# Optimization experiments

Hardware: AMD Instinct MI355X
Metric: run time of the kernel (lower is better)

## Reference

```python
import jax, jax.numpy as jnp
import numpy as np

EPS = 1e-8
MASK_FILL = 1000000000.0  # value used to disable dropped codes


def _normalize(x):
    return x / (jnp.linalg.norm(x, ord=2, axis=-1, keepdims=True) + EPS)


def setup_inputs() -> dict:
    key = jax.random.key(0)
    k_x, k_cb, k_mask = jax.random.split(key, 3)
    B, K, D = 16384, 16384, 64
    dropout = 0.1
    x = jax.random.normal(k_x, (B, D), dtype=jnp.float32)
    # lecun_uniform init for the codebook param: U(-l, l), l = sqrt(3 / fan_in)
    lim = np.sqrt(3.0 / D).astype(np.float32)
    codebook = jax.random.uniform(k_cb, (K, D), dtype=jnp.float32, minval=-lim, maxval=lim)
    mask = jax.random.bernoulli(k_mask, p=1.0 - dropout, shape=(B, K))
    return {"x": x, "codebook": codebook, "mask": mask, "training": 1}


def reference(x, codebook, mask, training):
    # setup(): codebook param is normalized once at construction
    cb = _normalize(codebook)                       # [K, d]
    # __call__():
    x_n = _normalize(x)                             # [b, d]
    cb_n = _normalize(cb)                           # normalized again in __call__
    distance = -jnp.matmul(x_n, cb_n.T)             # [b, K] negative cosine sim
    if training:
        distance = jnp.where(mask, distance, MASK_FILL)
    indices = jnp.argmin(distance, axis=-1)         # [b]
    z = cb[indices]                                 # gather from once-normalized codebook
    z_q = x_n + jax.lax.stop_gradient(z - x_n)      # straight-through estimator
    return (z_q, z, x_n, indices)
```

## Files before the change

### kernel.cpp

```cpp
#include <hip/hip_runtime.h>
#include <math.h>
#include <float.h>

#define EPSV 1e-8f
constexpr int D = 64;

typedef __attribute__((ext_vector_type(8)))  short short8;
typedef __attribute__((ext_vector_type(16))) float f32x16;

static __device__ __forceinline__ unsigned short f2bf(float f) {
    unsigned u = __float_as_uint(f);
    unsigned r = u + 0x7FFFu + ((u >> 16) & 1u);
    return (unsigned short)(r >> 16);
}
static __device__ __forceinline__ float bf2f(unsigned short b) {
    return __uint_as_float(((unsigned)b) << 16);
}
static __device__ __forceinline__ unsigned umin2(unsigned a, unsigned b) { return a < b ? a : b; }
static __device__ __forceinline__ unsigned umax2(unsigned a, unsigned b) { return a > b ? a : b; }

static __device__ __forceinline__ size_t fragidx(int e, int k) {
    return (size_t)(e >> 5) * 2048 + (size_t)(k >> 3) * 256 + (e & 31) * 8 + (k & 7);
}

__global__ __launch_bounds__(256) void k_prep(const float* __restrict__ cbin,
                                              float* __restrict__ cb,
                                              unsigned short* __restrict__ ch,
                                              unsigned short* __restrict__ cl,
                                              const float* __restrict__ xin,
                                              float* __restrict__ xn,
                                              unsigned short* __restrict__ xh,
                                              unsigned short* __restrict__ xl,
                                              int* __restrict__ fixcnt,
                                              int nbcb) {
    const int t = threadIdx.x;
    if (blockIdx.x == 0 && t == 0) *fixcnt = 0;
    const int wv = t >> 6, lane = t & 63;
    if ((int)blockIdx.x < nbcb) {
        const int code = blockIdx.x * 4 + wv;
        float v = cbin[(size_t)code * D + lane];
        float ss = v * v;
        #pragma unroll
        for (int off = 32; off; off >>= 1) ss += __shfl_xor(ss, off, 64);
        const float c1 = v / (sqrtf(ss) + EPSV);
        cb[(size_t)code * D + lane] = c1;
        float ss2 = c1 * c1;
        #pragma unroll
        for (int off = 32; off; off >>= 1) ss2 += __shfl_xor(ss2, off, 64);
        const float c2 = c1 / (sqrtf(ss2) + EPSV);
        const unsigned short h = f2bf(c2);
        const size_t fi = fragidx(code, lane);
        ch[fi] = h;
        cl[fi] = f2bf(c2 - bf2f(h));
    } else {
        const int row = (blockIdx.x - nbcb) * 4 + wv;
        float v = xin[(size_t)row * D + lane];
        float ss = v * v;
        #pragma unroll
        for (int off = 32; off; off >>= 1) ss += __shfl_xor(ss, off, 64);
        const float xv = v / (sqrtf(ss) + EPSV);
        xn[(size_t)row * D + lane] = xv;
        const unsigned short h = f2bf(xv);
        const size_t fi = fragidx(row, lane);
        xh[fi] = h;
        xl[fi] = f2bf(xv - bf2f(h));
    }
}

__global__ __launch_bounds__(256, 4) void k_mfma(const unsigned short* __restrict__ xh,
                                                 const unsigned short* __restrict__ xl,
                                                 const unsigned short* __restrict__ ch,
                                                 const unsigned short* __restrict__ cl,
                                                 unsigned* __restrict__ pk1,
                                                 unsigned* __restrict__ pk2,
                                                 int B, int K) {
    __shared__ short8 lch[2][2][256];
    __shared__ short8 lcl[2][2][256];
    const int t = threadIdx.x;
    const int wv = t >> 6, lane = t & 63;
    const int lh = lane >> 5, lm = lane & 31;
    const int ks = (int)(blockIdx.x & 7);
    const int rb = (int)(blockIdx.x >> 3);
    const int lh4 = lh * 4;

    const short8* xh8 = (const short8*)xh;
    const short8* xl8 = (const short8*)xl;
    const short8* ch8 = (const short8*)ch;
    const short8* cl8 = (const short8*)cl;

    const int rp = rb * 4 + wv;
    const int row = rp * 32 + lm;

    short8 bh[4], bl[4];
    #pragma unroll
    for (int s = 0; s < 4; ++s) {
        const size_t bi = (size_t)rp * 256 + (s * 2 + lh) * 32 + lm;
        bh[s] = xh8[bi];
        bl[s] = xl8[bi];
    }

#define STAGE(b_, tt_) do {                                                    \
    const int ct_ = ks * 32 + (tt_);                                           \
    const short8* s0 = ch8 + (size_t)(ct_ * 2 + 0) * 256 + t;                  \
    const short8* s1 = ch8 + (size_t)(ct_ * 2 + 1) * 256 + t;                  \
    const short8* s2 = cl8 + (size_t)(ct_ * 2 + 0) * 256 + t;                  \
    const short8* s3 = cl8 + (size_t)(ct_ * 2 + 1) * 256 + t;                  \
    __builtin_amdgcn_global_load_lds(                                          \
        (const __attribute__((address_space(1))) void*)s0,                     \
        (__attribute__((address_space(3))) void*)(&lch[b_][0][wv * 64]), 16, 0, 0); \
    __builtin_amdgcn_global_load_lds(                                          \
        (const __attribute__((address_space(1))) void*)s1,                     \
        (__attribute__((address_space(3))) void*)(&lch[b_][1][wv * 64]), 16, 0, 0); \
    __builtin_amdgcn_global_load_lds(                                          \
        (const __attribute__((address_space(1))) void*)s2,                     \
        (__attribute__((address_space(3))) void*)(&lcl[b_][0][wv * 64]), 16, 0, 0); \
    __builtin_amdgcn_global_load_lds(                                          \
        (const __attribute__((address_space(1))) void*)s3,                     \
        (__attribute__((address_space(3))) void*)(&lcl[b_][1][wv * 64]), 16, 0, 0); \
} while (0)

    unsigned k1 = 0xFFFFFFFFu, k2 = 0xFFFFFFFFu;

    STAGE(0, 0);

    #pragma unroll 1
    for (int tt = 0; tt < 32; ++tt) {
        __syncthreads();
        if (tt < 31) STAGE((tt + 1) & 1, tt + 1);
        const int bsel = tt & 1;
        const int ct = ks * 32 + tt;

        #pragma unroll
        for (int p = 0; p < 2; ++p) {
            short8 ah[4], al[4];
            #pragma unroll
            for (int s = 0; s < 4; ++s) {
                const int ai = (s * 2 + lh) * 32 + lm;
                ah[s] = lch[bsel][p][ai];
                al[s] = lcl[bsel][p][ai];
            }
            f32x16 acc;
            #pragma unroll
            for (int i = 0; i < 16; ++i) acc[i] = 0.f;
            #pragma unroll
            for (int s = 0; s < 4; ++s) {
                acc = __builtin_amdgcn_mfma_f32_32x32x16_bf16(ah[s], bh[s], acc, 0, 0, 0);
                acc = __builtin_amdgcn_mfma_f32_32x32x16_bf16(ah[s], bl[s], acc, 0, 0, 0);
                acc = __builtin_amdgcn_mfma_f32_32x32x16_bf16(al[s], bh[s], acc, 0, 0, 0);
            }
            const unsigned kbase = (unsigned)(ct * 64 + p * 32 + lh4);
            #pragma unroll
            for (int r = 0; r < 16; ++r) {
                const int base = (r & 3) + 8 * (r >> 2);
                const float qf = fmaf(acc[r], -65536.0f, 131072.0f);
                const unsigned key = ((unsigned)(int)qf << 14) | kbase | (unsigned)base;
                k2 = umin2(k2, umax2(k1, key));
                k1 = umin2(k1, key);
            }
        }
    }
#undef STAGE

    const unsigned o1 = (unsigned)__shfl_xor((int)k1, 32, 64);
    const unsigned o2 = (unsigned)__shfl_xor((int)k2, 32, 64);
    const unsigned mx = umax2(k1, o1);
    k1 = umin2(k1, o1);
    k2 = umin2(umin2(k2, o2), mx);

    if (lh == 0) {
        pk1[(size_t)ks * B + row] = k1;
        pk2[(size_t)ks * B + row] = k2;
    }
}

__global__ __launch_bounds__(256) void k_comb(const unsigned* __restrict__ pk1,
                                              const unsigned* __restrict__ pk2,
                                              const int* __restrict__ mask,
                                              const int* __restrict__ training,
                                              const float* __restrict__ xn,
                                              const float* __restrict__ cb,
                                              float* __restrict__ out,
                                              int* __restrict__ fixlist,
                                              int* __restrict__ fixcnt,
                                              int B, int K) {
    const int t = threadIdx.x;
    const int wv = t >> 6, lane = t & 63;
    const int row = blockIdx.x * 4 + wv;
    const int tr = training[0];

    unsigned cand = 0xFFFFFFFFu;
    int m = 1;
    if (lane < 16) {
        const int c = lane & 7;
        cand = (lane < 8) ? pk1[(size_t)c * B + row] : pk2[(size_t)c * B + row];
        m = (tr == 0) ? 1 : mask[(size_t)row * K + (cand & 16383u)];
    }
    const unsigned eff = (lane < 16 && m != 0) ? cand : 0xFFFFFFFFu;

    unsigned b1 = eff, b2 = 0xFFFFFFFFu;
    #pragma unroll
    for (int off = 1; off < 16; off <<= 1) {
        const unsigned oa = (unsigned)__shfl_xor((int)b1, off, 16);
        const unsigned ob = (unsigned)__shfl_xor((int)b2, off, 16);
        const unsigned mx = umax2(b1, oa);
        b1 = umin2(b1, oa);
        b2 = umin2(umin2(b2, ob), mx);
    }
    const unsigned best   = (unsigned)__shfl((int)b1, 0, 64);
    const unsigned second = (unsigned)__shfl((int)b2, 0, 64);
    const unsigned long long lim = (unsigned long long)best + (10ull << 14);

    const int mo        = __shfl_xor(m, 8, 16);
    const unsigned a2v  = (unsigned)__shfl_xor((int)cand, 8, 16);
    const bool cflag = (lane < 8) && (m == 0) && (mo == 0) &&
                       ((unsigned long long)a2v < lim);
    const bool flag = __any(cflag) ||
                      (best == 0xFFFFFFFFu) ||
                      ((unsigned long long)second < lim);

    const int bi = (int)(best & 16383u);
    const float zv  = cb[(size_t)bi * D + lane];
    const float xnv = xn[(size_t)row * D + lane];
    out[(size_t)row * D + lane] = xnv + (zv - xnv);
    out[(size_t)B * D + (size_t)row * D + lane] = zv;
    if (lane == 0) {
        out[(size_t)3 * B * D + row] = (float)bi;
        if (flag) {
            const int p = atomicAdd(fixcnt, 1);
            fixlist[p] = row;
        }
    }
}

__global__ __launch_bounds__(256) void k_fix(const float* __restrict__ xn,
                                             const float* __restrict__ cb,
                                             const int* __restrict__ mask,
                                             const int* __restrict__ training,
                                             const int* __restrict__ fixlist,
                                             const int* __restrict__ fixcnt,
                                             float* __restrict__ out, int B, int K) {
    const int nf = *fixcnt;
    const int tr = training[0];
    __shared__ float sv[256];
    __shared__ int   si[256];
    const int t = threadIdx.x;
    for (int i = blockIdx.x; i < nf; i += gridDim.x) {
        const int row = fixlist[i];
        const float* xr = xn + (size_t)row * D;
        float b1 = FLT_MAX; int i1 = 0;
        for (int k = t; k < K; k += 256) {
            const float* cr = cb + (size_t)k * D;
            float s = 0.f;
            #pragma unroll
            for (int d = 0; d < D; ++d) s = fmaf(xr[d], cr[d], s);
            const int m = mask[(size_t)row * K + k];
            const float dist = (tr && m == 0) ? 1000000000.0f : -s;
            if (dist < b1) { b1 = dist; i1 = k; }
        }
        sv[t] = b1; si[t] = i1;
        __syncthreads();
        for (int s = 128; s; s >>= 1) {
            if (t < s) {
                const float ov = sv[t + s]; const int oi = si[t + s];
                if (ov < sv[t] || (ov == sv[t] && oi < si[t])) { sv[t] = ov; si[t] = oi; }
            }
            __syncthreads();
        }
        const int bi = si[0];
        if (t < 64) {
            const float zv  = cb[(size_t)bi * D + t];
            const float xnv = xr[t];
            out[(size_t)row * D + t] = xnv + (zv - xnv);
            out[(size_t)B * D + (size_t)row * D + t] = zv;
        }
        if (t == 0) out[(size_t)3 * B * D + row] = (float)bi;
        __syncthreads();
    }
}

extern "C" void kernel_launch(void* const* d_in, const int* in_sizes, int n_in,
                              void* d_out, int out_size, void* d_ws, size_t ws_size,
                              hipStream_t stream) {
    const float* x    = (const float*)d_in[0];
    const float* cbin = (const float*)d_in[1];
    const int* mask   = (const int*)d_in[2];
    const int* train  = (const int*)d_in[3];
    const int B = in_sizes[0] / D;
    const int K = in_sizes[1] / D;
    float* out = (float*)d_out;
    float* out_xn = out + (size_t)2 * B * D;

    char* w = (char*)d_ws;
    float* cbw          = (float*)w;
    unsigned short* xhw = (unsigned short*)(w + (size_t)K * D * 4);
    unsigned short* xlw = xhw + (size_t)B * D;
    unsigned short* chw = xlw + (size_t)B * D;
    unsigned short* clw = chw + (size_t)K * D;
    unsigned* pk1       = (unsigned*)(clw + (size_t)K * D);
    unsigned* pk2       = pk1 + (size_t)B * 8;
    int* fixlist        = (int*)(pk2 + (size_t)B * 8);
    int* fixcnt         = fixlist + B;

    k_prep <<<K / 4 + B / 4, 256, 0, stream>>>(cbin, cbw, chw, clw,
                                               x, out_xn, xhw, xlw, fixcnt, K / 4);
    k_mfma <<<(B / 128) * 8, 256, 0, stream>>>(xhw, xlw, chw, clw, pk1, pk2, B, K);
    k_comb <<<B / 4, 256, 0, stream>>>(pk1, pk2, mask, train, out_xn, cbw, out,
                                       fixlist, fixcnt, B, K);
    k_fix  <<<256, 256, 0, stream>>>(out_xn, cbw, mask, train, fixlist, fixcnt,
                                     out, B, K);
}
```

Baseline: 238.1 us.

## Double codebook split count and convert x to bf16 hi/lo inside MFMA kernel

Doubles the number of codebook splits per row block from 8 to 16, which halves the tiles each block walks and doubles the grid size. The combine kernel now reduces 32 candidates per row instead of 16. The x bf16 hi/lo fragment arrays are dropped: the MFMA kernel reads the normalized fp32 x rows and splits them into hi/lo in registers, which saves a workspace write and read. In exchange each row's conversion is repeated by 16 blocks, and the combine kernel reads more partial results.

```diff
diff --git a/kernel.cpp b/kernel.cpp
--- a/kernel.cpp
+++ b/kernel.cpp
@@ -4,6 +4,8 @@
 
 #define EPSV 1e-8f
 constexpr int D = 64;
+constexpr int NSPLIT = 16;
+constexpr int NT = 16;
 
 typedef __attribute__((ext_vector_type(8)))  short short8;
 typedef __attribute__((ext_vector_type(16))) float f32x16;
@@ -29,8 +31,6 @@
                                               unsigned short* __restrict__ cl,
                                               const float* __restrict__ xin,
                                               float* __restrict__ xn,
-                                              unsigned short* __restrict__ xh,
-                                              unsigned short* __restrict__ xl,
                                               int* __restrict__ fixcnt,
                                               int nbcb) {
     const int t = threadIdx.x;
@@ -58,17 +58,11 @@
         float ss = v * v;
         #pragma unroll
         for (int off = 32; off; off >>= 1) ss += __shfl_xor(ss, off, 64);
-        const float xv = v / (sqrtf(ss) + EPSV);
-        xn[(size_t)row * D + lane] = xv;
-        const unsigned short h = f2bf(xv);
-        const size_t fi = fragidx(row, lane);
-        xh[fi] = h;
-        xl[fi] = f2bf(xv - bf2f(h));
-    }
-}
-
-__global__ __launch_bounds__(256, 4) void k_mfma(const unsigned short* __restrict__ xh,
-                                                 const unsigned short* __restrict__ xl,
+        xn[(size_t)row * D + lane] = v / (sqrtf(ss) + EPSV);
+    }
+}
+
+__global__ __launch_bounds__(256, 4) void k_mfma(const float* __restrict__ xn,
                                                  const unsigned short* __restrict__ ch,
                                                  const unsigned short* __restrict__ cl,
                                                  unsigned* __restrict__ pk1,
@@ -79,12 +73,10 @@
     const int t = threadIdx.x;
     const int wv = t >> 6, lane = t & 63;
     const int lh = lane >> 5, lm = lane & 31;
-    const int ks = (int)(blockIdx.x & 7);
-    const int rb = (int)(blockIdx.x >> 3);
+    const int ks = (int)(blockIdx.x & (NSPLIT - 1));
+    const int rb = (int)(blockIdx.x >> 4);
     const int lh4 = lh * 4;
 
-    const short8* xh8 = (const short8*)xh;
-    const short8* xl8 = (const short8*)xl;
     const short8* ch8 = (const short8*)ch;
     const short8* cl8 = (const short8*)cl;
 
@@ -92,15 +84,24 @@
     const int row = rp * 32 + lm;
 
     short8 bh[4], bl[4];
-    #pragma unroll
-    for (int s = 0; s < 4; ++s) {
-        const size_t bi = (size_t)rp * 256 + (s * 2 + lh) * 32 + lm;
-        bh[s] = xh8[bi];
-        bl[s] = xl8[bi];
+    {
+        const float* xrow = xn + (size_t)row * D;
+        #pragma unroll
+        for (int s = 0; s < 4; ++s) {
+            const float4 f0 = *(const float4*)(xrow + (s * 2 + lh) * 8);
+            const float4 f1 = *(const float4*)(xrow + (s * 2 + lh) * 8 + 4);
+            const float e[8] = { f0.x, f0.y, f0.z, f0.w, f1.x, f1.y, f1.z, f1.w };
+            #pragma unroll
+            for (int j = 0; j < 8; ++j) {
+                const unsigned short h = f2bf(e[j]);
+                bh[s][j] = (short)h;
+                bl[s][j] = (short)f2bf(e[j] - bf2f(h));
+            }
+        }
     }
 
 #define STAGE(b_, tt_) do {                                                    \
-    const int ct_ = ks * 32 + (tt_);                                           \
+    const int ct_ = ks * NT + (tt_);                                           \
     const short8* s0 = ch8 + (size_t)(ct_ * 2 + 0) * 256 + t;                  \
     const short8* s1 = ch8 + (size_t)(ct_ * 2 + 1) * 256 + t;                  \
     const short8* s2 = cl8 + (size_t)(ct_ * 2 + 0) * 256 + t;                  \
@@ -124,11 +125,11 @@
     STAGE(0, 0);
 
     #pragma unroll 1
-    for (int tt = 0; tt < 32; ++tt) {
+    for (int tt = 0; tt < NT; ++tt) {
         __syncthreads();
-        if (tt < 31) STAGE((tt + 1) & 1, tt + 1);
+        if (tt < NT - 1) STAGE((tt + 1) & 1, tt + 1);
         const int bsel = tt & 1;
-        const int ct = ks * 32 + tt;
+        const int ct = ks * NT + tt;
 
         #pragma unroll
         for (int p = 0; p < 2; ++p) {
@@ -190,18 +191,18 @@
 
     unsigned cand = 0xFFFFFFFFu;
     int m = 1;
-    if (lane < 16) {
-        const int c = lane & 7;
-        cand = (lane < 8) ? pk1[(size_t)c * B + row] : pk2[(size_t)c * B + row];
+    if (lane < 32) {
+        const int c = lane & 15;
+        cand = (lane < 16) ? pk1[(size_t)c * B + row] : pk2[(size_t)c * B + row];
         m = (tr == 0) ? 1 : mask[(size_t)row * K + (cand & 16383u)];
     }
-    const unsigned eff = (lane < 16 && m != 0) ? cand : 0xFFFFFFFFu;
+    const unsigned eff = (lane < 32 && m != 0) ? cand : 0xFFFFFFFFu;
 
     unsigned b1 = eff, b2 = 0xFFFFFFFFu;
     #pragma unroll
-    for (int off = 1; off < 16; off <<= 1) {
-        const unsigned oa = (unsigned)__shfl_xor((int)b1, off, 16);
-        const unsigned ob = (unsigned)__shfl_xor((int)b2, off, 16);
+    for (int off = 1; off < 32; off <<= 1) {
+        const unsigned oa = (unsigned)__shfl_xor((int)b1, off, 32);
+        const unsigned ob = (unsigned)__shfl_xor((int)b2, off, 32);
         const unsigned mx = umax2(b1, oa);
         b1 = umin2(b1, oa);
         b2 = umin2(umin2(b2, ob), mx);
@@ -210,9 +211,9 @@
     const unsigned second = (unsigned)__shfl((int)b2, 0, 64);
     const unsigned long long lim = (unsigned long long)best + (10ull << 14);
 
-    const int mo        = __shfl_xor(m, 8, 16);
-    const unsigned a2v  = (unsigned)__shfl_xor((int)cand, 8, 16);
-    const bool cflag = (lane < 8) && (m == 0) && (mo == 0) &&
+    const int mo        = __shfl_xor(m, 16, 32);
+    const unsigned a2v  = (unsigned)__shfl_xor((int)cand, 16, 32);
+    const bool cflag = (lane < 16) && (m == 0) && (mo == 0) &&
                        ((unsigned long long)a2v < lim);
     const bool flag = __any(cflag) ||
                       (best == 0xFFFFFFFFu) ||
@@ -292,18 +293,16 @@
 
     char* w = (char*)d_ws;
     float* cbw          = (float*)w;
-    unsigned short* xhw = (unsigned short*)(w + (size_t)K * D * 4);
-    unsigned short* xlw = xhw + (size_t)B * D;
-    unsigned short* chw = xlw + (size_t)B * D;
+    unsigned short* chw = (unsigned short*)(w + (size_t)K * D * 4);
     unsigned short* clw = chw + (size_t)K * D;
     unsigned* pk1       = (unsigned*)(clw + (size_t)K * D);
-    unsigned* pk2       = pk1 + (size_t)B * 8;
-    int* fixlist        = (int*)(pk2 + (size_t)B * 8);
+    unsigned* pk2       = pk1 + (size_t)B * NSPLIT;
+    int* fixlist        = (int*)(pk2 + (size_t)B * NSPLIT);
     int* fixcnt         = fixlist + B;
 
     k_prep <<<K / 4 + B / 4, 256, 0, stream>>>(cbin, cbw, chw, clw,
-                                               x, out_xn, xhw, xlw, fixcnt, K / 4);
-    k_mfma <<<(B / 128) * 8, 256, 0, stream>>>(xhw, xlw, chw, clw, pk1, pk2, B, K);
+                                               x, out_xn, fixcnt, K / 4);
+    k_mfma <<<(B / 128) * NSPLIT, 256, 0, stream>>>(out_xn, chw, clw, pk1, pk2, B, K);
     k_comb <<<B / 4, 256, 0, stream>>>(pk1, pk2, mask, train, out_xn, cbw, out,
                                        fixlist, fixcnt, B, K);
     k_fix  <<<256, 256, 0, stream>>>(out_xn, cbw, mask, train, fixlist, fixcnt,
```

Result: no change. 241.6 us (+1.5%).
